# Performance work log

Measured on AMD Instinct MI355X. Metric: run time of the kernel, lower is better.

Reference implementation:

```python
import jax, jax.numpy as jnp
import numpy as np

INPUT_DIM = 32
HIDDEN = 512
ACTION_DIM = 4
NUM_OBJ = 10
BATCH = 1024
LN_EPS = 1e-5


def _edge_list(B, K):
    # fully connected, no self loops, row-major like torch.nonzero
    adj = np.ones((K, K), dtype=np.int64) - np.eye(K, dtype=np.int64)
    e = np.argwhere(adj)                      # [K*(K-1), 2]
    e = np.tile(e, (B, 1))
    off = np.repeat(np.arange(B, dtype=np.int64) * K, K * (K - 1))
    e = e + off[:, None]
    return jnp.asarray(e[:, 0]), jnp.asarray(e[:, 1])  # row, col


def _layer_norm(x, g, b):
    m = x.mean(-1, keepdims=True)
    v = x.var(-1, keepdims=True)
    return (x - m) / jnp.sqrt(v + LN_EPS) * g + b


def _mlp(x, w1, b1, w2, b2, g, bt, w3, b3):
    h = jax.nn.relu(x @ w1 + b1)
    h = jax.nn.relu(_layer_norm(h @ w2 + b2, g, bt))
    return h @ w3 + b3


def setup_inputs() -> dict:
    key = jax.random.key(0)
    ks = jax.random.split(key, 16)

    def lin(k, i, o):
        return jax.random.normal(k, (i, o), jnp.float32) / np.sqrt(i)

    states = jax.random.normal(ks[0], (BATCH, NUM_OBJ, INPUT_DIM), jnp.float32)
    action = jax.random.randint(ks[1], (BATCH,), 0, ACTION_DIM, jnp.int64)

    node_in = HIDDEN + INPUT_DIM + ACTION_DIM  # 548
    return {
        "states": states, "action": action,
        # edge MLP: 2*input_dim -> hidden
        "ew1": lin(ks[2], 2 * INPUT_DIM, HIDDEN), "eb1": jnp.zeros((HIDDEN,), jnp.float32),
        "ew2": lin(ks[3], HIDDEN, HIDDEN),        "eb2": jnp.zeros((HIDDEN,), jnp.float32),
        "eg": jnp.ones((HIDDEN,), jnp.float32),   "ebt": jnp.zeros((HIDDEN,), jnp.float32),
        "ew3": lin(ks[4], HIDDEN, HIDDEN),        "eb3": jnp.zeros((HIDDEN,), jnp.float32),
        # node MLP: (input + action + hidden) -> input_dim
        "nw1": lin(ks[5], node_in, HIDDEN),       "nb1": jnp.zeros((HIDDEN,), jnp.float32),
        "nw2": lin(ks[6], HIDDEN, HIDDEN),        "nb2": jnp.zeros((HIDDEN,), jnp.float32),
        "ng": jnp.ones((HIDDEN,), jnp.float32),   "nbt": jnp.zeros((HIDDEN,), jnp.float32),
        "nw3": lin(ks[7], HIDDEN, INPUT_DIM),     "nb3": jnp.zeros((INPUT_DIM,), jnp.float32),
    }


def reference(states, action, ew1, eb1, ew2, eb2, eg, ebt, ew3, eb3,
              nw1, nb1, nw2, nb2, ng, nbt, nw3, nb3):
    B, K, D = states.shape
    node_attr = states.reshape(-1, D)                      # [B*K, D]

    row, col = _edge_list(B, K)
    edge_in = jnp.concatenate([node_attr[row], node_attr[col]], axis=1)  # [E, 2D]
    edge_attr = _mlp(edge_in, ew1, eb1, ew2, eb2, eg, ebt, ew3, eb3)     # [E, H]
    agg = jax.ops.segment_sum(edge_attr, row, num_segments=B * K)       # [B*K, H]

    # copy_action=True, 1-D action: one-hot, same vector for each object
    oh = jax.nn.one_hot(action, ACTION_DIM, dtype=jnp.float32)          # [B, A]
    action_vec = jnp.tile(oh, (1, K)).reshape(-1, ACTION_DIM)           # [B*K, A]

    node_in = jnp.concatenate([node_attr, action_vec, agg], axis=1)     # [B*K, D+A+H]
    out = _mlp(node_in, nw1, nb1, nw2, nb2, ng, nbt, nw3, nb3)          # [B*K, D]
    return out.reshape(B, K, D)
```

## Files before the change

kernel.cpp:

```cpp
#include <hip/hip_runtime.h>


#define HID 512
#define DIN 32
#define KOBJ 10
#define NGRAPH 1024
#define NNODES (NGRAPH*KOBJ)
#define NEDGE (NGRAPH*90)
#define NBLK (NEDGE/64)
#define LN_EPS 1e-5f

typedef __bf16 bf16x8 __attribute__((ext_vector_type(8)));
typedef unsigned short u16x8 __attribute__((ext_vector_type(8)));
typedef unsigned short u16x4 __attribute__((ext_vector_type(4)));
typedef float f32x4 __attribute__((ext_vector_type(4)));

__device__ __forceinline__ unsigned short f2bf(float f) {
    unsigned u = __builtin_bit_cast(unsigned, f);
    u += 0x7fffu + ((u >> 16) & 1u);
    return (unsigned short)(u >> 16);
}
__device__ __forceinline__ float bf2f(unsigned short h) {
    unsigned u = ((unsigned)h) << 16;
    return __builtin_bit_cast(float, u);
}
__device__ __forceinline__ void gl_lds16(const void* g, void* l) {
    __builtin_amdgcn_global_load_lds(
        (__attribute__((address_space(1))) void*)g,
        (__attribute__((address_space(3))) void*)l, 16, 0, 0);
}

__global__ void megapack(const float* __restrict__ ew1, const float* __restrict__ ew2,
                         const float* __restrict__ nw1, const float* __restrict__ nw2,
                         unsigned short* __restrict__ ew1p, unsigned short* __restrict__ ew2p,
                         unsigned short* __restrict__ nw1p, unsigned short* __restrict__ nw2p)
{
    int idx = blockIdx.x * 256 + threadIdx.x;
    if (idx < 32768) {
        int j = idx & 7, c = (idx >> 3) & 1023, kb = idx >> 13;
        int k = kb * 8 + j;
        float v = (c < 512) ? ew1[(size_t)k * 512 + c]
                            : ew1[(size_t)(32 + k) * 512 + (c - 512)];
        ew1p[idx] = f2bf(v);
    } else if (idx < 32768 + 262144) {
        int i = idx - 32768;
        int j = i & 7, c = (i >> 3) & 511, kb = i >> 12;
        ew2p[i] = f2bf(ew2[(size_t)(kb * 8 + j) * 512 + c]);
    } else if (idx < 294912 + 294912) {
        int i = idx - 294912;
        int j = i & 7, c = (i >> 3) & 511, kb = i >> 12;
        int k = kb * 8 + j;
        int sk = (k < 36) ? k : (k < 64 ? -1 : k - 28);
        nw1p[i] = f2bf(sk < 0 ? 0.f : nw1[(size_t)sk * 512 + c]);
    } else if (idx < 589824 + 262144) {
        int i = idx - 589824;
        int j = i & 7, c = (i >> 3) & 511, kb = i >> 12;
        nw2p[i] = f2bf(nw2[(size_t)(kb * 8 + j) * 512 + c]);
    }
}

__global__ __launch_bounds__(512) void fold_w2(
    const float* __restrict__ ew3, const unsigned short* __restrict__ nw1p,
    const float* __restrict__ nw1, const float* __restrict__ nb1,
    const float* __restrict__ eb3, unsigned short* __restrict__ Wfp,
    float* __restrict__ nbf)
{
    if (blockIdx.x == 32) {
        int c = threadIdx.x;
        if (c < 512) {
            float s = 0.f;
            for (int m = 0; m < 512; ++m)
                s = fmaf(eb3[m], nw1[(size_t)(36 + m) * 512 + c], s);
            nbf[c] = nb1[c] + 9.f * s;
        }
        return;
    }
    const int t = threadIdx.x, w = t >> 6, lane = t & 63;
    const int lr = lane & 15, lg = lane >> 4;
    const int rb = blockIdx.x * 16;
    f32x4 acc[4] = {};
    for (int kc = 0; kc < 16; ++kc) {
        const float* s = ew3 + (size_t)(rb + lr) * 512 + kc * 32 + lg * 8;
        float4 x0 = *(const float4*)s, x1 = *(const float4*)(s + 4);
        u16x8 u;
        u[0] = f2bf(x0.x); u[1] = f2bf(x0.y); u[2] = f2bf(x0.z); u[3] = f2bf(x0.w);
        u[4] = f2bf(x1.x); u[5] = f2bf(x1.y); u[6] = f2bf(x1.z); u[7] = f2bf(x1.w);
        bf16x8 a = __builtin_bit_cast(bf16x8, u);
        const size_t kb = (size_t)(8 + kc * 4 + lg) * 512;
#pragma unroll
        for (int nt = 0; nt < 4; ++nt) {
            int c = w * 64 + nt * 16 + lr;
            bf16x8 b = __builtin_bit_cast(bf16x8, *(const u16x8*)(nw1p + (kb + c) * 8));
            acc[nt] = __builtin_amdgcn_mfma_f32_16x16x32_bf16(a, b, acc[nt], 0, 0, 0);
        }
    }
#pragma unroll
    for (int reg = 0; reg < 4; ++reg)
#pragma unroll
        for (int nt = 0; nt < 4; ++nt) {
            int k = rb + lg * 4 + reg;
            int c = w * 64 + nt * 16 + lr;
            Wfp[((size_t)(k >> 3) * 512 + c) * 8 + (k & 7)] = f2bf(acc[nt][reg]);
        }
}

__global__ __launch_bounds__(256) void pq_xa(
    const float* __restrict__ X, const int* __restrict__ act,
    const unsigned short* __restrict__ ew1p, const unsigned short* __restrict__ nw1p,
    const float* __restrict__ eb1, const float* __restrict__ nbf,
    unsigned short* __restrict__ PQ, unsigned short* __restrict__ Rb)
{
    const int t = threadIdx.x, w = t >> 6, lane = t & 63;
    const int lr = lane & 15, lg = lane >> 4;
    const int rb = blockIdx.x * 32;
    const int mode = blockIdx.y;

    bf16x8 a[2];
#pragma unroll
    for (int m = 0; m < 2; ++m) {
        const float* s = X + (size_t)(rb + m * 16 + lr) * 32 + lg * 8;
        float4 x0 = *(const float4*)s, x1 = *(const float4*)(s + 4);
        u16x8 u;
        u[0] = f2bf(x0.x); u[1] = f2bf(x0.y); u[2] = f2bf(x0.z); u[3] = f2bf(x0.w);
        u[4] = f2bf(x1.x); u[5] = f2bf(x1.y); u[6] = f2bf(x1.z); u[7] = f2bf(x1.w);
        a[m] = __builtin_bit_cast(bf16x8, u);
    }

    if (mode < 2) {
        const int half = mode;
        f32x4 acc[2][8] = {};
#pragma unroll
        for (int nt = 0; nt < 8; ++nt) {
            int col = half * 512 + w * 128 + nt * 16 + lr;
            bf16x8 b = __builtin_bit_cast(bf16x8, *(const u16x8*)(ew1p + ((size_t)lg * 1024 + col) * 8));
            acc[0][nt] = __builtin_amdgcn_mfma_f32_16x16x32_bf16(a[0], b, acc[0][nt], 0, 0, 0);
            acc[1][nt] = __builtin_amdgcn_mfma_f32_16x16x32_bf16(a[1], b, acc[1][nt], 0, 0, 0);
        }
#pragma unroll
        for (int nt = 0; nt < 8; ++nt) {
            int col = w * 128 + nt * 16 + lr;
            float eb = (half == 0) ? eb1[col] : 0.f;
#pragma unroll
            for (int m = 0; m < 2; ++m)
#pragma unroll
                for (int reg = 0; reg < 4; ++reg)
                    PQ[(size_t)(rb + m * 16 + lg * 4 + reg) * 1024 + half * 512 + col]
                        = f2bf(acc[m][nt][reg] + eb);
        }
    } else {
        bf16x8 a1[2];
#pragma unroll
        for (int m = 0; m < 2; ++m) {
            int row = rb + m * 16 + lr;
            u16x8 v = (u16x8)(unsigned short)0;
            if (lg == 0) {
                int ac = act[row / KOBJ];
                v[ac & 3] = (unsigned short)0x3f80;
            }
            a1[m] = __builtin_bit_cast(bf16x8, v);
        }
        f32x4 acc[2][8] = {};
#pragma unroll
        for (int nt = 0; nt < 8; ++nt) {
            int col = w * 128 + nt * 16 + lr;
            bf16x8 b0 = __builtin_bit_cast(bf16x8, *(const u16x8*)(nw1p + ((size_t)lg * 512 + col) * 8));
            bf16x8 b1 = __builtin_bit_cast(bf16x8, *(const u16x8*)(nw1p + ((size_t)(4 + lg) * 512 + col) * 8));
#pragma unroll
            for (int m = 0; m < 2; ++m) {
                acc[m][nt] = __builtin_amdgcn_mfma_f32_16x16x32_bf16(a[m], b0, acc[m][nt], 0, 0, 0);
                acc[m][nt] = __builtin_amdgcn_mfma_f32_16x16x32_bf16(a1[m], b1, acc[m][nt], 0, 0, 0);
            }
        }
#pragma unroll
        for (int nt = 0; nt < 8; ++nt) {
            int col = w * 128 + nt * 16 + lr;
            float bb = nbf[col];
#pragma unroll
            for (int m = 0; m < 2; ++m)
#pragma unroll
                for (int reg = 0; reg < 4; ++reg)
                    Rb[(size_t)(rb + m * 16 + lg * 4 + reg) * 512 + col]
                        = f2bf(acc[m][nt][reg] + bb);
        }
    }
}

__global__ __launch_bounds__(512, 4) void edge_v15(
    const unsigned short* __restrict__ PQ, const unsigned short* __restrict__ ew2p,
    const float* __restrict__ eb2, const float* __restrict__ eg,
    const float* __restrict__ ebt, unsigned short* __restrict__ Spart)
{
    __shared__ __align__(16) char ldsraw[77824];
    __shared__ float sums[64], ssums[64];
    unsigned short* Hcol = (unsigned short*)ldsraw;

    const int t = threadIdx.x, w = t >> 6, lane = t & 63;
    const int lr = lane & 15, lg = lane >> 4;
    const int wr = w >> 2, wc = w & 3;
    const int rb = blockIdx.x * 64;

    if (t < 64) { sums[t] = 0.f; ssums[t] = 0.f; }

    const bool ab = (t < 256);
    const int arow = t >> 2, akg = t & 3;
    const int e = rb + arow;
    const int g = e / 90, le = e - g * 90;
    const int i = le / 9, jj = le - i * 9;
    const int j = jj + (jj >= i);
    const unsigned short* pqP = PQ + ((size_t)(g * KOBJ + i)) * 1024 + akg * 8;
    const unsigned short* pqQ = PQ + ((size_t)(g * KOBJ + j)) * 1024 + 512 + akg * 8;

    u16x8 rp = (u16x8)(unsigned short)0, rq = (u16x8)(unsigned short)0;
    auto loadPQ = [&](int kc) {
        if (ab) {
            rp = *(const u16x8*)(pqP + kc * 32);
            rq = *(const u16x8*)(pqQ + kc * 32);
        }
    };
    auto buildA = [&](int buf) {
        if (ab) {
            u16x8 o;
#pragma unroll
            for (int q = 0; q < 8; ++q)
                o[q] = f2bf(fmaxf(bf2f(rp[q]) + bf2f(rq[q]), 0.f));
            *(u16x8*)(ldsraw + 65536 + buf * 5120 + arow * 80 + akg * 16) = o;
        }
    };
    auto fillB = [&](int kc, int buf) {
        char* Bb = ldsraw + buf * 32768;
#pragma unroll
        for (int RR = 0; RR < 4; ++RR)
            gl_lds16(ew2p + (size_t)kc * 16384 + RR * 4096 + t * 8, Bb + RR * 8192 + w * 1024);
    };

    f32x4 acc[2][8] = {};
    loadPQ(0); buildA(0); loadPQ(1); fillB(0, 0);
    __syncthreads();
    int cur = 0;
    for (int kc = 0; kc < 16; ++kc) {
        if (kc < 15) {
            fillB(kc + 1, cur ^ 1);
            buildA(cur ^ 1);
            if (kc < 14) loadPQ(kc + 2);
        }
        const unsigned short* Ab = (const unsigned short*)(ldsraw + 65536 + cur * 5120);
        const unsigned short* Bb = (const unsigned short*)(ldsraw + cur * 32768);
        bf16x8 a0 = *(const bf16x8*)(Ab + (wr * 32 + lr) * 40 + lg * 8);
        bf16x8 a1 = *(const bf16x8*)(Ab + (wr * 32 + 16 + lr) * 40 + lg * 8);
#pragma unroll
        for (int nt = 0; nt < 8; ++nt) {
            bf16x8 b = *(const bf16x8*)(Bb + ((size_t)lg * 512 + wc * 128 + nt * 16 + lr) * 8);
            acc[0][nt] = __builtin_amdgcn_mfma_f32_16x16x32_bf16(a0, b, acc[0][nt], 0, 0, 0);
            acc[1][nt] = __builtin_amdgcn_mfma_f32_16x16x32_bf16(a1, b, acc[1][nt], 0, 0, 0);
        }
        __syncthreads();
        cur ^= 1;
    }

    float b2[8], gv[8], bb[8];
#pragma unroll
    for (int nt = 0; nt < 8; ++nt) {
        int c = wc * 128 + nt * 16 + lr;
        b2[nt] = eb2[c]; gv[nt] = eg[c]; bb[nt] = ebt[c];
    }
#pragma unroll
    for (int m = 0; m < 2; ++m)
#pragma unroll
        for (int reg = 0; reg < 4; ++reg) {
            float s = 0.f, ss = 0.f;
#pragma unroll
            for (int nt = 0; nt < 8; ++nt) {
                float v = acc[m][nt][reg] + b2[nt];
                acc[m][nt][reg] = v;
                s += v; ss += v * v;
            }
#pragma unroll
            for (int msk = 1; msk < 16; msk <<= 1) {
                s  += __shfl_xor(s,  msk, 64);
                ss += __shfl_xor(ss, msk, 64);
            }
            if (lr == 0) {
                int rl = wr * 32 + m * 16 + lg * 4 + reg;
                atomicAdd(&sums[rl], s);
                atomicAdd(&ssums[rl], ss);
            }
        }
    __syncthreads();

#pragma unroll
    for (int m = 0; m < 2; ++m)
#pragma unroll
        for (int nt = 0; nt < 8; ++nt) {
            int c = wc * 128 + nt * 16 + lr;
            u16x4 o;
#pragma unroll
            for (int reg = 0; reg < 4; ++reg) {
                int rl = wr * 32 + m * 16 + lg * 4 + reg;
                float mean = sums[rl] * (1.f / 512.f);
                float var  = ssums[rl] * (1.f / 512.f) - mean * mean;
                float inv  = rsqrtf(var + LN_EPS);
                float h = fmaxf((acc[m][nt][reg] - mean) * inv * gv[nt] + bb[nt], 0.f);
                o[reg] = f2bf(h);
            }
            *(u16x4*)(&Hcol[c * 72 + wr * 32 + m * 16 + lg * 4]) = o;
        }
    __syncthreads();

    {
        const int n0 = rb / 9;
        f32x4 sacc[4] = {};
#pragma unroll
        for (int kc2 = 0; kc2 < 2; ++kc2) {
            u16x8 ia;
#pragma unroll
            for (int q = 0; q < 8; ++q) {
                int k = kc2 * 32 + lg * 8 + q;
                int node = (rb + k) / 9 - n0;
                ia[q] = (node == lr) ? (unsigned short)0x3F80 : (unsigned short)0;
            }
            bf16x8 af = __builtin_bit_cast(bf16x8, ia);
#pragma unroll
            for (int nt = 0; nt < 4; ++nt) {
                int c = w * 64 + nt * 16 + lr;
                bf16x8 bf = *(const bf16x8*)(&Hcol[c * 72 + kc2 * 32 + lg * 8]);
                sacc[nt] = __builtin_amdgcn_mfma_f32_16x16x32_bf16(af, bf, sacc[nt], 0, 0, 0);
            }
        }
        if (lg < 2) {
            unsigned short* dst = Spart + (size_t)blockIdx.x * 4096;
#pragma unroll
            for (int nt = 0; nt < 4; ++nt)
#pragma unroll
                for (int reg = 0; reg < 4; ++reg) {
                    int node = lg * 4 + reg;
                    int c = w * 64 + nt * 16 + lr;
                    dst[node * 512 + c] = f2bf(sacc[nt][reg]);
                }
        }
    }
}

__global__ __launch_bounds__(256) void gather_s(
    const unsigned short* __restrict__ Spart, unsigned short* __restrict__ S)
{
    int idx = blockIdx.x * 256 + threadIdx.x;
    int n = idx >> 6, c8 = idx & 63;
    int e0 = 9 * n;
    int b1 = e0 >> 6, b2 = (e0 + 8) >> 6;
    int nl1 = n - (b1 * 64) / 9;
    const unsigned short* p1 = Spart + ((size_t)b1 * 8 + nl1) * 512 + c8 * 8;
    u16x8 v1 = *(const u16x8*)p1;
    float x[8];
#pragma unroll
    for (int q = 0; q < 8; ++q) x[q] = bf2f(v1[q]);
    if (b2 != b1) {
        int nl2 = n - (b2 * 64) / 9;
        const unsigned short* p2 = Spart + ((size_t)b2 * 8 + nl2) * 512 + c8 * 8;
        u16x8 v2 = *(const u16x8*)p2;
#pragma unroll
        for (int q = 0; q < 8; ++q) x[q] += bf2f(v2[q]);
    }
    u16x8 o;
#pragma unroll
    for (int q = 0; q < 8; ++q) o[q] = f2bf(x[q]);
    *(u16x8*)(S + (size_t)n * 512 + c8 * 8) = o;
}

__global__ __launch_bounds__(512, 4) void node_hh(
    const unsigned short* __restrict__ S, const unsigned short* __restrict__ Wfp,
    const unsigned short* __restrict__ Rb, unsigned short* __restrict__ Hh)
{
    __shared__ __align__(16) unsigned short Bt[32768];
    __shared__ __align__(16) unsigned short At[2048];
    const int t = threadIdx.x, w = t >> 6, lane = t & 63;
    const int lr = lane & 15, lg = lane >> 4;
    const int rb = blockIdx.x * 32;

    f32x4 acc[2][4] = {};
    for (int kc = 0; kc < 8; ++kc) {
        __syncthreads();
#pragma unroll
        for (int RR = 0; RR < 8; ++RR)
            gl_lds16(Wfp + ((size_t)kc * 4096 + RR * 512 + t) * 8,
                     (char*)Bt + RR * 8192 + w * 1024);
        if (w < 4) {
            int row = t >> 3, cp = t & 7;
            int scol = cp ^ (row & 7);
            gl_lds16(S + (size_t)(rb + row) * 512 + kc * 64 + scol * 8,
                     (char*)At + (t & ~63) * 16);
        }
        __syncthreads();
#pragma unroll
        for (int ks = 0; ks < 2; ++ks) {
            int kidx = ks * 4 + lg;
            bf16x8 a0 = *(const bf16x8*)(At + ( 0 + lr) * 64 + (kidx ^ (lr & 7)) * 8);
            bf16x8 a1 = *(const bf16x8*)(At + (16 + lr) * 64 + (kidx ^ (lr & 7)) * 8);
#pragma unroll
            for (int nt = 0; nt < 4; ++nt) {
                bf16x8 b = *(const bf16x8*)(Bt + ((size_t)kidx * 512 + w * 64 + nt * 16 + lr) * 8);
                acc[0][nt] = __builtin_amdgcn_mfma_f32_16x16x32_bf16(a0, b, acc[0][nt], 0, 0, 0);
                acc[1][nt] = __builtin_amdgcn_mfma_f32_16x16x32_bf16(a1, b, acc[1][nt], 0, 0, 0);
            }
        }
    }
#pragma unroll
    for (int m = 0; m < 2; ++m)
#pragma unroll
        for (int reg = 0; reg < 4; ++reg) {
            int row = rb + m * 16 + lg * 4 + reg;
#pragma unroll
            for (int nt = 0; nt < 4; ++nt) {
                int c = w * 64 + nt * 16 + lr;
                float v = acc[m][nt][reg] + bf2f(Rb[(size_t)row * 512 + c]);
                Hh[(size_t)row * 512 + c] = f2bf(fmaxf(v, 0.f));
            }
        }
}

__global__ __launch_bounds__(512, 4) void node_ln(
    const unsigned short* __restrict__ A, const unsigned short* __restrict__ Wp,
    const float* __restrict__ bias, const float* __restrict__ gamma,
    const float* __restrict__ beta, unsigned short* __restrict__ outb)
{
    __shared__ __align__(16) unsigned short Bt[32768];
    __shared__ __align__(16) unsigned short At[2048];
    __shared__ float sums[32], ssums[32];
    const int t = threadIdx.x, w = t >> 6, lane = t & 63;
    const int lr = lane & 15, lg = lane >> 4;
    const int rb = blockIdx.x * 32;
    if (t < 32) { sums[t] = 0.f; ssums[t] = 0.f; }

    f32x4 acc[2][4] = {};
    for (int kc = 0; kc < 8; ++kc) {
        __syncthreads();
#pragma unroll
        for (int RR = 0; RR < 8; ++RR)
            gl_lds16(Wp + ((size_t)kc * 4096 + RR * 512 + t) * 8,
                     (char*)Bt + RR * 8192 + w * 1024);
        if (w < 4) {
            int row = t >> 3, cp = t & 7;
            int scol = cp ^ (row & 7);
            gl_lds16(A + (size_t)(rb + row) * 512 + kc * 64 + scol * 8,
                     (char*)At + (t & ~63) * 16);
        }
        __syncthreads();
#pragma unroll
        for (int ks = 0; ks < 2; ++ks) {
            int kidx = ks * 4 + lg;
            bf16x8 a0 = *(const bf16x8*)(At + ( 0 + lr) * 64 + (kidx ^ (lr & 7)) * 8);
            bf16x8 a1 = *(const bf16x8*)(At + (16 + lr) * 64 + (kidx ^ (lr & 7)) * 8);
#pragma unroll
            for (int nt = 0; nt < 4; ++nt) {
                bf16x8 b = *(const bf16x8*)(Bt + ((size_t)kidx * 512 + w * 64 + nt * 16 + lr) * 8);
                acc[0][nt] = __builtin_amdgcn_mfma_f32_16x16x32_bf16(a0, b, acc[0][nt], 0, 0, 0);
                acc[1][nt] = __builtin_amdgcn_mfma_f32_16x16x32_bf16(a1, b, acc[1][nt], 0, 0, 0);
            }
        }
    }

    float bv[4], gv[4], be[4];
#pragma unroll
    for (int nt = 0; nt < 4; ++nt) {
        int c = w * 64 + nt * 16 + lr;
        bv[nt] = bias[c]; gv[nt] = gamma[c]; be[nt] = beta[c];
    }
#pragma unroll
    for (int m = 0; m < 2; ++m)
#pragma unroll
        for (int reg = 0; reg < 4; ++reg) {
            float s = 0.f, ss = 0.f;
#pragma unroll
            for (int nt = 0; nt < 4; ++nt) {
                float v = acc[m][nt][reg] + bv[nt];
                acc[m][nt][reg] = v;
                s += v; ss += v * v;
            }
#pragma unroll
            for (int msk = 1; msk < 16; msk <<= 1) {
                s  += __shfl_xor(s,  msk, 64);
                ss += __shfl_xor(ss, msk, 64);
            }
            if (lr == 0) {
                atomicAdd(&sums [m * 16 + lg * 4 + reg], s);
                atomicAdd(&ssums[m * 16 + lg * 4 + reg], ss);
            }
        }
    __syncthreads();
#pragma unroll
    for (int m = 0; m < 2; ++m)
#pragma unroll
        for (int reg = 0; reg < 4; ++reg) {
            int rl = m * 16 + lg * 4 + reg;
            float mean = sums[rl] * (1.f / 512.f);
            float var  = ssums[rl] * (1.f / 512.f) - mean * mean;
            float inv  = rsqrtf(var + LN_EPS);
#pragma unroll
            for (int nt = 0; nt < 4; ++nt) {
                float v = fmaxf((acc[m][nt][reg] - mean) * inv * gv[nt] + be[nt], 0.f);
                outb[(size_t)(rb + rl) * 512 + w * 64 + nt * 16 + lr] = f2bf(v);
            }
        }
}

__global__ __launch_bounds__(256) void out_v4(
    const unsigned short* __restrict__ H2, const float* __restrict__ W3,
    const float* __restrict__ b3, float* __restrict__ out)
{
    int t = threadIdx.x;
    int r = blockIdx.x * 8 + (t >> 5);
    int c = t & 31;
    const unsigned short* h = H2 + (size_t)r * HID;
    float acc = 0.f;
#pragma unroll 8
    for (int k8 = 0; k8 < 64; ++k8) {
        u16x8 hv = *(const u16x8*)(h + k8 * 8);
#pragma unroll
        for (int q = 0; q < 8; ++q)
            acc = fmaf(bf2f(hv[q]), W3[(k8 * 8 + q) * DIN + c], acc);
    }
    out[(size_t)r * DIN + c] = acc + b3[c];
}

extern "C" void kernel_launch(void* const* d_in, const int* in_sizes, int n_in,
                              void* d_out, int out_size, void* d_ws, size_t ws_size,
                              hipStream_t stream)
{
    const float* states = (const float*)d_in[0];
    const int*   action = (const int*)d_in[1];
    const float* ew1 = (const float*)d_in[2];
    const float* eb1 = (const float*)d_in[3];
    const float* ew2 = (const float*)d_in[4];
    const float* eb2 = (const float*)d_in[5];
    const float* eg  = (const float*)d_in[6];
    const float* ebt = (const float*)d_in[7];
    const float* ew3 = (const float*)d_in[8];
    const float* eb3 = (const float*)d_in[9];
    const float* nw1 = (const float*)d_in[10];
    const float* nb1 = (const float*)d_in[11];
    const float* nw2 = (const float*)d_in[12];
    const float* nb2 = (const float*)d_in[13];
    const float* ng  = (const float*)d_in[14];
    const float* nbt = (const float*)d_in[15];
    const float* nw3 = (const float*)d_in[16];
    const float* nb3 = (const float*)d_in[17];

    char* wsb = (char*)d_ws;
    unsigned short* PQ    = (unsigned short*)(wsb);
    unsigned short* Spart = (unsigned short*)(wsb + 20971520);
    unsigned short* S     = (unsigned short*)(wsb + 32768000);
    unsigned short* Rb    = (unsigned short*)(wsb + 43253760);
    unsigned short* Hh    = (unsigned short*)(wsb + 53739520);
    unsigned short* H2    = (unsigned short*)(wsb + 64225280);
    unsigned short* ew1p  = (unsigned short*)(wsb + 74711040);
    unsigned short* ew2p  = (unsigned short*)(wsb + 74776576);
    unsigned short* nw1p  = (unsigned short*)(wsb + 75300864);
    unsigned short* nw2p  = (unsigned short*)(wsb + 75890688);
    unsigned short* Wfp   = (unsigned short*)(wsb + 76414976);
    float*          nbf   = (float*)         (wsb + 76939264);
    float* out = (float*)d_out;

    hipLaunchKernelGGL(megapack, dim3(3328), dim3(256), 0, stream,
                       ew1, ew2, nw1, nw2, ew1p, ew2p, nw1p, nw2p);
    hipLaunchKernelGGL(fold_w2, dim3(33), dim3(512), 0, stream,
                       ew3, nw1p, nw1, nb1, eb3, Wfp, nbf);
    hipLaunchKernelGGL(pq_xa, dim3(320, 3), dim3(256), 0, stream,
                       states, action, ew1p, nw1p, eb1, nbf, PQ, Rb);
    hipLaunchKernelGGL(edge_v15, dim3(NBLK), dim3(512), 0, stream,
                       PQ, ew2p, eb2, eg, ebt, Spart);
    hipLaunchKernelGGL(gather_s, dim3(NNODES * 64 / 256), dim3(256), 0, stream, Spart, S);
    hipLaunchKernelGGL(node_hh, dim3(320), dim3(512), 0, stream, S, Wfp, Rb, Hh);
    hipLaunchKernelGGL(node_ln, dim3(320), dim3(512), 0, stream, Hh, nw2p, nb2, ng, nbt, H2);
    hipLaunchKernelGGL(out_v4, dim3(NNODES / 8), dim3(256), 0, stream, H2, nw3, nb3, out);
}
```

Measured before the change: 194.0 us.

## Fuse final node linear layer into LayerNorm kernel using MFMA

Merges the output projection (512->32) into the node LayerNorm kernel. The normalized activations are staged in shared memory, multiplied against a newly packed bf16 nw3 with MFMA, and the per-wave partial sums are reduced through LDS before writing the output. This removes the H2 round trip through global memory and one kernel launch. In exchange it adds extra syncs and a slightly larger shared-memory footprint per block, and the contraction now runs on bf16 weights.

```diff
diff --git a/kernel.cpp b/kernel.cpp
--- a/kernel.cpp
+++ b/kernel.cpp
@@ -1,5 +1,4 @@
 #include <hip/hip_runtime.h>
-
 
 #define HID 512
 #define DIN 32
@@ -32,8 +31,10 @@
 
 __global__ void megapack(const float* __restrict__ ew1, const float* __restrict__ ew2,
                          const float* __restrict__ nw1, const float* __restrict__ nw2,
+                         const float* __restrict__ nw3,
                          unsigned short* __restrict__ ew1p, unsigned short* __restrict__ ew2p,
-                         unsigned short* __restrict__ nw1p, unsigned short* __restrict__ nw2p)
+                         unsigned short* __restrict__ nw1p, unsigned short* __restrict__ nw2p,
+                         unsigned short* __restrict__ nw3p)
 {
     int idx = blockIdx.x * 256 + threadIdx.x;
     if (idx < 32768) {
@@ -56,6 +57,10 @@
         int i = idx - 589824;
         int j = i & 7, c = (i >> 3) & 511, kb = i >> 12;
         nw2p[i] = f2bf(nw2[(size_t)(kb * 8 + j) * 512 + c]);
+    } else if (idx < 851968 + 16384) {
+        int i = idx - 851968;
+        int j = i & 7, c2 = (i >> 3) & 31, kb = i >> 8;
+        nw3p[i] = f2bf(nw3[(size_t)(kb * 8 + j) * 32 + c2]);
     }
 }
 
@@ -417,14 +422,16 @@
         }
 }
 
-__global__ __launch_bounds__(512, 4) void node_ln(
+__global__ __launch_bounds__(512, 4) void node_lo(
     const unsigned short* __restrict__ A, const unsigned short* __restrict__ Wp,
     const float* __restrict__ bias, const float* __restrict__ gamma,
-    const float* __restrict__ beta, unsigned short* __restrict__ outb)
-{
-    __shared__ __align__(16) unsigned short Bt[32768];
-    __shared__ __align__(16) unsigned short At[2048];
+    const float* __restrict__ beta, const unsigned short* __restrict__ nw3p,
+    const float* __restrict__ nb3, float* __restrict__ out)
+{
+    __shared__ __align__(16) char raw[69632];
     __shared__ float sums[32], ssums[32];
+    unsigned short* Bt = (unsigned short*)raw;
+    unsigned short* At = (unsigned short*)(raw + 65536);
     const int t = threadIdx.x, w = t >> 6, lane = t & 63;
     const int lr = lane & 15, lg = lane >> 4;
     const int rb = blockIdx.x * 32;
@@ -436,12 +443,12 @@
 #pragma unroll
         for (int RR = 0; RR < 8; ++RR)
             gl_lds16(Wp + ((size_t)kc * 4096 + RR * 512 + t) * 8,
-                     (char*)Bt + RR * 8192 + w * 1024);
+                     raw + RR * 8192 + w * 1024);
         if (w < 4) {
             int row = t >> 3, cp = t & 7;
             int scol = cp ^ (row & 7);
             gl_lds16(A + (size_t)(rb + row) * 512 + kc * 64 + scol * 8,
-                     (char*)At + (t & ~63) * 16);
+                     raw + 65536 + (t & ~63) * 16);
         }
         __syncthreads();
 #pragma unroll
@@ -486,6 +493,8 @@
             }
         }
     __syncthreads();
+
+    unsigned short* Hst = (unsigned short*)raw;
 #pragma unroll
     for (int m = 0; m < 2; ++m)
 #pragma unroll
@@ -496,29 +505,51 @@
             float inv  = rsqrtf(var + LN_EPS);
 #pragma unroll
             for (int nt = 0; nt < 4; ++nt) {
-                float v = fmaxf((acc[m][nt][reg] - mean) * inv * gv[nt] + be[nt], 0.f);
-                outb[(size_t)(rb + rl) * 512 + w * 64 + nt * 16 + lr] = f2bf(v);
-            }
-        }
-}
-
-__global__ __launch_bounds__(256) void out_v4(
-    const unsigned short* __restrict__ H2, const float* __restrict__ W3,
-    const float* __restrict__ b3, float* __restrict__ out)
-{
-    int t = threadIdx.x;
-    int r = blockIdx.x * 8 + (t >> 5);
-    int c = t & 31;
-    const unsigned short* h = H2 + (size_t)r * HID;
-    float acc = 0.f;
-#pragma unroll 8
-    for (int k8 = 0; k8 < 64; ++k8) {
-        u16x8 hv = *(const u16x8*)(h + k8 * 8);
-#pragma unroll
-        for (int q = 0; q < 8; ++q)
-            acc = fmaf(bf2f(hv[q]), W3[(k8 * 8 + q) * DIN + c], acc);
-    }
-    out[(size_t)r * DIN + c] = acc + b3[c];
+                int c = w * 64 + nt * 16 + lr;
+                float v = fmaxf((acc[m][reg * 0 + nt][reg] * 0.f + acc[m][nt][reg] - mean) * inv * gv[nt] + be[nt], 0.f);
+                Hst[rl * 520 + c] = f2bf(v);
+            }
+        }
+    __syncthreads();
+
+    float* Pp = (float*)(raw + 34816);
+    {
+        f32x4 acc2[2][2] = {};
+#pragma unroll
+        for (int kc3 = 0; kc3 < 2; ++kc3) {
+            int kbase = w * 64 + kc3 * 32;
+            bf16x8 a0 = *(const bf16x8*)(Hst + ( 0 + lr) * 520 + kbase + lg * 8);
+            bf16x8 a1 = *(const bf16x8*)(Hst + (16 + lr) * 520 + kbase + lg * 8);
+#pragma unroll
+            for (int ntt = 0; ntt < 2; ++ntt) {
+                int kb = (kbase >> 3) + lg;
+                bf16x8 b = __builtin_bit_cast(bf16x8,
+                    *(const u16x8*)(nw3p + ((size_t)kb * 32 + ntt * 16 + lr) * 8));
+                acc2[0][ntt] = __builtin_amdgcn_mfma_f32_16x16x32_bf16(a0, b, acc2[0][ntt], 0, 0, 0);
+                acc2[1][ntt] = __builtin_amdgcn_mfma_f32_16x16x32_bf16(a1, b, acc2[1][ntt], 0, 0, 0);
+            }
+        }
+        __syncthreads();
+#pragma unroll
+        for (int mt = 0; mt < 2; ++mt)
+#pragma unroll
+            for (int ntt = 0; ntt < 2; ++ntt)
+#pragma unroll
+                for (int reg = 0; reg < 4; ++reg) {
+                    int row = mt * 16 + lg * 4 + reg;
+                    int col = ntt * 16 + lr;
+                    Pp[(size_t)w * 1024 + row * 32 + col] = acc2[mt][ntt][reg];
+                }
+    }
+    __syncthreads();
+
+    for (int e2 = t; e2 < 1024; e2 += 512) {
+        int row = e2 >> 5, col = e2 & 31;
+        float s = 0.f;
+#pragma unroll
+        for (int ww = 0; ww < 8; ++ww) s += Pp[(size_t)ww * 1024 + e2];
+        out[(size_t)(rb + row) * 32 + col] = s + nb3[col];
+    }
 }
 
 extern "C" void kernel_launch(void* const* d_in, const int* in_sizes, int n_in,
@@ -550,17 +581,17 @@
     unsigned short* S     = (unsigned short*)(wsb + 32768000);
     unsigned short* Rb    = (unsigned short*)(wsb + 43253760);
     unsigned short* Hh    = (unsigned short*)(wsb + 53739520);
-    unsigned short* H2    = (unsigned short*)(wsb + 64225280);
     unsigned short* ew1p  = (unsigned short*)(wsb + 74711040);
     unsigned short* ew2p  = (unsigned short*)(wsb + 74776576);
     unsigned short* nw1p  = (unsigned short*)(wsb + 75300864);
     unsigned short* nw2p  = (unsigned short*)(wsb + 75890688);
     unsigned short* Wfp   = (unsigned short*)(wsb + 76414976);
     float*          nbf   = (float*)         (wsb + 76939264);
+    unsigned short* nw3p  = (unsigned short*)(wsb + 76941312);
     float* out = (float*)d_out;
 
-    hipLaunchKernelGGL(megapack, dim3(3328), dim3(256), 0, stream,
-                       ew1, ew2, nw1, nw2, ew1p, ew2p, nw1p, nw2p);
+    hipLaunchKernelGGL(megapack, dim3(3392), dim3(256), 0, stream,
+                       ew1, ew2, nw1, nw2, nw3, ew1p, ew2p, nw1p, nw2p, nw3p);
     hipLaunchKernelGGL(fold_w2, dim3(33), dim3(512), 0, stream,
                        ew3, nw1p, nw1, nb1, eb3, Wfp, nbf);
     hipLaunchKernelGGL(pq_xa, dim3(320, 3), dim3(256), 0, stream,
@@ -569,6 +600,6 @@
                        PQ, ew2p, eb2, eg, ebt, Spart);
     hipLaunchKernelGGL(gather_s, dim3(NNODES * 64 / 256), dim3(256), 0, stream, Spart, S);
     hipLaunchKernelGGL(node_hh, dim3(320), dim3(512), 0, stream, S, Wfp, Rb, Hh);
-    hipLaunchKernelGGL(node_ln, dim3(320), dim3(512), 0, stream, Hh, nw2p, nb2, ng, nbt, H2);
-    hipLaunchKernelGGL(out_v4, dim3(NNODES / 8), dim3(256), 0, stream, H2, nw3, nb3, out);
-}
+    hipLaunchKernelGGL(node_lo, dim3(320), dim3(512), 0, stream,
+                       Hh, nw2p, nb2, ng, nbt, nw3p, nb3, out);
+}
```

New measurement: 165.0 us. 15.0% less time.
